# Kernel optimization log

Measured on AMD Instinct MI355X. Metric: run time of the kernel, lower is better.

The kernel has to match this reference:

```python
import jax, jax.numpy as jnp
import numpy as np

K = 16          # neighbors per node
EPS = 1e-5      # BatchNorm eps
BN_SCALE = 1.0 / np.sqrt(1.0 + EPS)  # eval BN with running mean=0, var=1


def _knn_idx(x, k):
    # x: [B, N, d] -> idx [B, N, k] of k nearest neighbors (self excluded)
    sq = jnp.sum(x * x, axis=-1)                               # [B, N]
    d2 = sq[:, :, None] + sq[:, None, :] - 2.0 * jnp.einsum('bnd,bmd->bnm', x, x)
    n = x.shape[1]
    d2 = jnp.where(jnp.eye(n, dtype=bool)[None], jnp.inf, d2)  # no self loops
    _, idx = jax.lax.top_k(-d2, k)
    return idx


def _edge_conv(x, idx, W, b, g, be):
    # PyG EdgeConv: max_j MLP([x_i, x_j - x_i]); MLP = Linear+BN(eval)+ReLU
    xj = jax.vmap(lambda xb, ib: xb[ib])(x, idx)               # [B, N, k, d]
    xi = x[:, :, None, :]
    m = jnp.concatenate([jnp.broadcast_to(xi, xj.shape), xj - xi], axis=-1)
    h = m @ W + b                                              # [B, N, k, out]
    h = g * (h * BN_SCALE) + be                                # eval BatchNorm
    h = jax.nn.relu(h)
    return jnp.max(h, axis=2)                                  # scatter-max over k


def setup_inputs() -> dict:
    key = jax.random.key(0)
    ks = jax.random.split(key, 16)
    B, N, D, C = 128, 256, 6, 12

    def w(k_, shape, fan_in):
        return (jax.random.normal(k_, shape, jnp.float32) / np.sqrt(fan_in)).astype(jnp.float32)

    inp = {
        'x':   jax.random.normal(ks[0], (B, N, D), jnp.float32),
        'W1':  w(ks[1], (2 * 6, 64), 12),   'b1': jnp.zeros((64,), jnp.float32),
        'g1':  jnp.ones((64,), jnp.float32), 'be1': jnp.zeros((64,), jnp.float32),
        'W2':  w(ks[2], (2 * 64, 128), 128), 'b2': jnp.zeros((128,), jnp.float32),
        'g2':  jnp.ones((128,), jnp.float32), 'be2': jnp.zeros((128,), jnp.float32),
        'W3':  w(ks[3], (2 * 128, 256), 256), 'b3': jnp.zeros((256,), jnp.float32),
        'g3':  jnp.ones((256,), jnp.float32), 'be3': jnp.zeros((256,), jnp.float32),
        'Wf1': w(ks[4], (256, 128), 256),    'bf1': jnp.zeros((128,), jnp.float32),
        'gf':  jnp.ones((128,), jnp.float32), 'bef': jnp.zeros((128,), jnp.float32),
        'Wf2': w(ks[5], (128, C), 128),      'bf2': jnp.zeros((C,), jnp.float32),
    }
    return inp


def reference(x, W1, b1, g1, be1, W2, b2, g2, be2, W3, b3, g3, be3,
              Wf1, bf1, gf, bef, Wf2, bf2):
    h = _edge_conv(x, _knn_idx(x, K), W1, b1, g1, be1)   # [B, N, 64]
    h = _edge_conv(h, _knn_idx(h, K), W2, b2, g2, be2)   # [B, N, 128]
    h = _edge_conv(h, _knn_idx(h, K), W3, b3, g3, be3)   # [B, N, 256]
    p = jnp.max(h, axis=1)                               # global_max_pool [B, 256]
    f = jax.nn.relu(gf * ((p @ Wf1 + bf1) * BN_SCALE) + bef)
    return f @ Wf2 + bf2                                 # [B, num_classes]
```

## Files before the change

kernel.cpp:

```cpp
#include <hip/hip_runtime.h>
#include <cstdint>
#include <cstddef>

#define KNN 16
#define NPTS 256
#define NBATCH 128

static constexpr float BN_SCALE_F = 0.9999950000374997f;

__device__ inline unsigned int f32_ord(float f) {
    unsigned int u = __float_as_uint(f);
    return (u & 0x80000000u) ? ~u : (u | 0x80000000u);
}

__device__ __forceinline__ int wmap(int n) { return n + 4 * (n >> 4); }

template<int D>
__global__ __launch_bounds__(256) void sq_kernel(const float* __restrict__ x,
                                                 float* __restrict__ sq) {
    const int t = blockIdx.x * 256 + threadIdx.x;
    const float* r = x + (size_t)t * D;
    float s = 0.f;
    #pragma unroll
    for (int d = 0; d < D; ++d) s = fmaf(r[d], r[d], s);
    sq[t] = s;
}

template<int D>
__global__ __launch_bounds__(256) void knn_fused_kernel(
        const float* __restrict__ x, const float* __restrict__ sq,
        int* __restrict__ idx) {
    constexpr int KS = (D >= 16) ? 16 : D;
    const int t  = threadIdx.x;
    const int tx = t & 15, ty = t >> 4;
    const int sr = t >> 2, sc = t & 3;
    const int b  = blockIdx.x >> 2;
    const int i0 = (blockIdx.x & 3) * 64;
    const int base = b * NPTS;

    __shared__ float As[KS][68];
    __shared__ float Bs[KS][68];
    __shared__ float d2L[64][65];
    __shared__ unsigned short Mi[64][68];

    unsigned int Lv[16], Li[16];
    #pragma unroll
    for (int q = 0; q < 16; ++q) { Lv[q] = 0xFFFFFFFFu; Li[q] = 0u; }

    for (int jt = 0; jt < 4; ++jt) {
        const int j0 = jt * 64;
        float acc[4][4] = {};
        for (int k0 = 0; k0 < D; k0 += KS) {
            if constexpr (D % 16 == 0) {
                const int r  = t >> 2;
                const int cq = (t & 3) * 4;
                const float4 va = *(const float4*)(x + (size_t)(base + i0 + r) * D + k0 + cq);
                const float4 vb = *(const float4*)(x + (size_t)(base + j0 + r) * D + k0 + cq);
                As[cq + 0][r] = va.x; As[cq + 1][r] = va.y;
                As[cq + 2][r] = va.z; As[cq + 3][r] = va.w;
                Bs[cq + 0][r] = vb.x; Bs[cq + 1][r] = vb.y;
                Bs[cq + 2][r] = vb.z; Bs[cq + 3][r] = vb.w;
            } else {
                for (int e = t; e < 64 * KS; e += 256) {
                    const int r = e / KS, c = e % KS;
                    As[c][r] = x[(size_t)(base + i0 + r) * D + k0 + c];
                    Bs[c][r] = x[(size_t)(base + j0 + r) * D + k0 + c];
                }
            }
            __syncthreads();
            #pragma unroll
            for (int kk = 0; kk < KS; ++kk) {
                const float4 av = *(const float4*)&As[kk][ty * 4];
                const float4 bv = *(const float4*)&Bs[kk][tx * 4];
                const float am[4] = {av.x, av.y, av.z, av.w};
                const float bm[4] = {bv.x, bv.y, bv.z, bv.w};
                #pragma unroll
                for (int m = 0; m < 4; ++m)
                    #pragma unroll
                    for (int n = 0; n < 4; ++n)
                        acc[m][n] = fmaf(am[m], bm[n], acc[m][n]);
            }
            __syncthreads();
        }

        float sqi[4], sqj[4];
        #pragma unroll
        for (int m = 0; m < 4; ++m) {
            sqi[m] = sq[base + i0 + ty * 4 + m];
            sqj[m] = sq[base + j0 + tx * 4 + m];
        }
        #pragma unroll
        for (int m = 0; m < 4; ++m) {
            const int gi = i0 + ty * 4 + m;
            #pragma unroll
            for (int n = 0; n < 4; ++n) {
                float v = (sqi[m] + sqj[n]) - 2.f * acc[m][n];
                if (gi == j0 + tx * 4 + n) v = INFINITY;
                d2L[ty * 4 + m][tx * 4 + n] = v;
            }
        }
        __syncthreads();

        #pragma unroll
        for (int i = 0; i < 16; ++i) {
            const unsigned int v = f32_ord(d2L[sr][sc * 16 + i]);
            const unsigned int j = (unsigned int)(j0 + sc * 16 + i);
            #pragma unroll
            for (int q = 15; q >= 1; --q) {
                const bool a = v < Lv[q];
                const bool c = v < Lv[q - 1];
                Lv[q] = a ? (c ? Lv[q - 1] : v) : Lv[q];
                Li[q] = a ? (c ? Li[q - 1] : j) : Li[q];
            }
            const bool a0 = v < Lv[0];
            Lv[0] = a0 ? v : Lv[0];
            Li[0] = a0 ? j : Li[0];
        }
    }

    __syncthreads();
    #pragma unroll
    for (int q = 0; q < 16; ++q) {
        d2L[sr][sc * 16 + q] = __uint_as_float(Lv[q]);
        Mi[sr][sc * 16 + q]  = (unsigned short)Li[q];
    }
    __syncthreads();

    if (t < 64) {
        const int row = t;
        int h[4];
        unsigned int cv[4], ci[4];
        #pragma unroll
        for (int c = 0; c < 4; ++c) {
            h[c]  = 0;
            cv[c] = __float_as_uint(d2L[row][c * 16]);
            ci[c] = Mi[row][c * 16];
        }
        int outj[16];
        #pragma unroll
        for (int rd = 0; rd < 16; ++rd) {
            unsigned int bv = cv[0], bi = ci[0];
            int bc = 0;
            #pragma unroll
            for (int c = 1; c < 4; ++c) {
                const bool tk = (cv[c] < bv) | ((cv[c] == bv) & (ci[c] < bi));
                bv = tk ? cv[c] : bv;
                bi = tk ? ci[c] : bi;
                bc = tk ? c     : bc;
            }
            outj[rd] = (int)bi;
            #pragma unroll
            for (int c = 0; c < 4; ++c) {
                if (c == bc) {
                    const int hn = h[c] + 1;
                    h[c] = hn;
                    if (hn < 16) {
                        cv[c] = __float_as_uint(d2L[row][c * 16 + hn]);
                        ci[c] = Mi[row][c * 16 + hn];
                    } else {
                        cv[c] = 0xFFFFFFFFu;
                    }
                }
            }
        }
        int4* op = (int4*)(idx + (size_t)(base + i0 + row) * KNN);
        op[0] = make_int4(outj[0],  outj[1],  outj[2],  outj[3]);
        op[1] = make_int4(outj[4],  outj[5],  outj[6],  outj[7]);
        op[2] = make_int4(outj[8],  outj[9],  outj[10], outj[11]);
        op[3] = make_int4(outj[12], outj[13], outj[14], outj[15]);
    }
}

template<int D, int C>
__global__ __launch_bounds__(256) void mlp_gemm_kernel(
        const float* __restrict__ x, const float* __restrict__ W,
        const float* __restrict__ bias, const float* __restrict__ g,
        const float* __restrict__ be,
        float* __restrict__ A, float* __restrict__ Bv) {
    constexpr int BM = 128;
    constexpr int KT = (D >= 16) ? 16 : D;
    const int t  = threadIdx.x;
    const int m0 = blockIdx.x * BM;
    const int n0 = blockIdx.y * 128;
    const int tx = t & 15;
    const int ty = t >> 4;

    __shared__ float Xs[KT][BM + 4];
    __shared__ float Ws[KT][160];

    float acc[8][8] = {};

    for (int k0 = 0; k0 < D; k0 += KT) {
        if constexpr (D % 16 == 0) {
            const int r  = t >> 1;
            const int cq = (t & 1) * 8;
            const float* src = x + (size_t)(m0 + r) * D + k0 + cq;
            const float4 v0 = *(const float4*)(src);
            const float4 v1 = *(const float4*)(src + 4);
            Xs[cq + 0][r] = v0.x; Xs[cq + 1][r] = v0.y;
            Xs[cq + 2][r] = v0.z; Xs[cq + 3][r] = v0.w;
            Xs[cq + 4][r] = v1.x; Xs[cq + 5][r] = v1.y;
            Xs[cq + 6][r] = v1.z; Xs[cq + 7][r] = v1.w;
        } else {
            for (int e = t; e < BM * KT; e += 256) {
                const int r = e / KT, c = e % KT;
                Xs[c][r] = x[(size_t)(m0 + r) * D + k0 + c];
            }
        }
        if constexpr (D % 16 == 0) {
            const int wk = t >> 4;
            const int nq = (t & 15) * 8;
            const int mb = wmap(nq);
            const int gn = n0 + nq;
            const int kr = k0 + wk;
            if (gn < C) {
                const float* pt = W + (size_t)kr * C + gn;
                const float* pb = W + (size_t)(D + kr) * C + gn;
                const float4 t0 = *(const float4*)(pt);
                const float4 t1 = *(const float4*)(pt + 4);
                const float4 b0 = *(const float4*)(pb);
                const float4 b1 = *(const float4*)(pb + 4);
                *(float4*)&Ws[wk][mb]     = make_float4(t0.x - b0.x, t0.y - b0.y,
                                                        t0.z - b0.z, t0.w - b0.w);
                *(float4*)&Ws[wk][mb + 4] = make_float4(t1.x - b1.x, t1.y - b1.y,
                                                        t1.z - b1.z, t1.w - b1.w);
            } else {
                const float* pb = W + (size_t)(D + kr) * C + (gn - C);
                *(float4*)&Ws[wk][mb]     = *(const float4*)(pb);
                *(float4*)&Ws[wk][mb + 4] = *(const float4*)(pb + 4);
            }
        } else {
            for (int e = t; e < KT * 128; e += 256) {
                const int k = e >> 7, n = e & 127;
                const int gn = n0 + n, kr = k0 + k;
                Ws[k][wmap(n)] = (gn < C)
                    ? W[(size_t)kr * C + gn] - W[(size_t)(D + kr) * C + gn]
                    : W[(size_t)(D + kr) * C + (gn - C)];
            }
        }
        __syncthreads();

        const int mc = wmap(tx * 8);
        #pragma unroll
        for (int kk = 0; kk < KT; ++kk) {
            float xm[8], wn[8];
            *(float4*)&xm[0] = *(const float4*)&Xs[kk][ty * 8];
            *(float4*)&xm[4] = *(const float4*)&Xs[kk][ty * 8 + 4];
            *(float4*)&wn[0] = *(const float4*)&Ws[kk][mc];
            *(float4*)&wn[4] = *(const float4*)&Ws[kk][mc + 4];
            #pragma unroll
            for (int m = 0; m < 8; ++m)
                #pragma unroll
                for (int n = 0; n < 8; ++n)
                    acc[m][n] = fmaf(xm[m], wn[n], acc[m][n]);
        }
        __syncthreads();
    }

    const int gn = n0 + tx * 8;
    if (gn < C) {
        float fac[8];
        #pragma unroll
        for (int e = 0; e < 8; ++e) fac[e] = g[gn + e] * BN_SCALE_F;
        #pragma unroll
        for (int m = 0; m < 8; ++m) {
            float o[8];
            #pragma unroll
            for (int e = 0; e < 8; ++e) o[e] = fac[e] * acc[m][e];
            float* dst = A + (size_t)(m0 + ty * 8 + m) * C + gn;
            *(float4*)(dst)     = make_float4(o[0], o[1], o[2], o[3]);
            *(float4*)(dst + 4) = make_float4(o[4], o[5], o[6], o[7]);
        }
    } else {
        const int cb = gn - C;
        float fac[8], bb[8], bee[8];
        #pragma unroll
        for (int e = 0; e < 8; ++e) {
            fac[e] = g[cb + e] * BN_SCALE_F;
            bb[e]  = bias[cb + e];
            bee[e] = be[cb + e];
        }
        #pragma unroll
        for (int m = 0; m < 8; ++m) {
            float o[8];
            #pragma unroll
            for (int e = 0; e < 8; ++e)
                o[e] = fmaf(fac[e], acc[m][e] + bb[e], bee[e]);
            float* dst = Bv + (size_t)(m0 + ty * 8 + m) * C + cb;
            *(float4*)(dst)     = make_float4(o[0], o[1], o[2], o[3]);
            *(float4*)(dst + 4) = make_float4(o[4], o[5], o[6], o[7]);
        }
    }
}

template<int C>
__global__ __launch_bounds__(C) void combine_kernel(
        const float* A, const float* __restrict__ Bv,
        const int* __restrict__ idx, float* out) {
    const int bi = blockIdx.x;
    const int c  = threadIdx.x;
    __shared__ int nbr[KNN];
    if (c < KNN) nbr[c] = idx[(size_t)bi * KNN + c];
    __syncthreads();
    const int b0 = bi & ~255;
    float mx = -INFINITY;
    #pragma unroll
    for (int kk = 0; kk < KNN; ++kk)
        mx = fmaxf(mx, Bv[(size_t)(b0 + nbr[kk]) * C + c]);
    float a = A[(size_t)bi * C + c];
    out[(size_t)bi * C + c] = fmaxf(a + mx, 0.f);
}

__global__ __launch_bounds__(256) void head_kernel(
        const float* __restrict__ h3, const float* __restrict__ Wf1,
        const float* __restrict__ bf1, const float* __restrict__ gf,
        const float* __restrict__ bef, const float* __restrict__ Wf2,
        const float* __restrict__ bf2, float* __restrict__ out) {
    const int b   = blockIdx.x;
    const int tid = threadIdx.x;
    __shared__ float p[256];
    __shared__ float f[128];
    const float* hb = h3 + (size_t)b * NPTS * 256;
    float mx = -INFINITY;
    for (int n = 0; n < NPTS; ++n) mx = fmaxf(mx, hb[(size_t)n * 256 + tid]);
    p[tid] = mx;
    __syncthreads();
    if (tid < 128) {
        float acc = bf1[tid];
        for (int d = 0; d < 256; ++d)
            acc = fmaf(p[d], Wf1[(size_t)d * 128 + tid], acc);
        float v = gf[tid] * (acc * BN_SCALE_F) + bef[tid];
        f[tid] = fmaxf(v, 0.f);
    }
    __syncthreads();
    if (tid < 12) {
        float acc = bf2[tid];
        for (int d = 0; d < 128; ++d)
            acc = fmaf(f[d], Wf2[(size_t)d * 12 + tid], acc);
        out[(size_t)b * 12 + tid] = acc;
    }
}

extern "C" void kernel_launch(void* const* d_in, const int* in_sizes, int n_in,
                              void* d_out, int out_size, void* d_ws, size_t ws_size,
                              hipStream_t stream) {
    const float* x   = (const float*)d_in[0];
    const float* W1  = (const float*)d_in[1];
    const float* b1  = (const float*)d_in[2];
    const float* g1  = (const float*)d_in[3];
    const float* be1 = (const float*)d_in[4];
    const float* W2  = (const float*)d_in[5];
    const float* b2  = (const float*)d_in[6];
    const float* g2  = (const float*)d_in[7];
    const float* be2 = (const float*)d_in[8];
    const float* W3  = (const float*)d_in[9];
    const float* b3  = (const float*)d_in[10];
    const float* g3  = (const float*)d_in[11];
    const float* be3 = (const float*)d_in[12];
    const float* Wf1 = (const float*)d_in[13];
    const float* bf1 = (const float*)d_in[14];
    const float* gf  = (const float*)d_in[15];
    const float* bef = (const float*)d_in[16];
    const float* Wf2 = (const float*)d_in[17];
    const float* bf2 = (const float*)d_in[18];
    float* out = (float*)d_out;

    char* ws = (char*)d_ws;
    const size_t idx_bytes = (size_t)NBATCH * NPTS * KNN * sizeof(int);
    const size_t reg_bytes = (size_t)NBATCH * NPTS * 256 * sizeof(float);
    int*   idx = (int*)ws;
    float* R1  = (float*)(ws + idx_bytes);
    float* R2  = (float*)(ws + idx_bytes + reg_bytes);
    float* R3  = (float*)(ws + idx_bytes + 2 * reg_bytes);
    float* sqb = (float*)(ws + idx_bytes + 3 * reg_bytes);

    const int BN = NBATCH * NPTS;
    const int KNN_GRID = NBATCH * 4;
    const int MB = BN / 128;

    sq_kernel<6><<<BN / 256, 256, 0, stream>>>(x, sqb);
    knn_fused_kernel<6><<<KNN_GRID, 256, 0, stream>>>(x, sqb, idx);
    mlp_gemm_kernel<6, 64><<<dim3(MB, 1), 256, 0, stream>>>(
        x, W1, b1, g1, be1, R1, R2);
    combine_kernel<64><<<BN, 64, 0, stream>>>(R1, R2, idx, R1);

    sq_kernel<64><<<BN / 256, 256, 0, stream>>>(R1, sqb);
    knn_fused_kernel<64><<<KNN_GRID, 256, 0, stream>>>(R1, sqb, idx);
    mlp_gemm_kernel<64, 128><<<dim3(MB, 2), 256, 0, stream>>>(
        R1, W2, b2, g2, be2, R2, R3);
    combine_kernel<128><<<BN, 128, 0, stream>>>(R2, R3, idx, R2);

    sq_kernel<128><<<BN / 256, 256, 0, stream>>>(R2, sqb);
    knn_fused_kernel<128><<<KNN_GRID, 256, 0, stream>>>(R2, sqb, idx);
    mlp_gemm_kernel<128, 256><<<dim3(MB, 4), 256, 0, stream>>>(
        R2, W3, b3, g3, be3, R3, R1);
    combine_kernel<256><<<BN, 256, 0, stream>>>(R3, R1, idx, R3);

    head_kernel<<<NBATCH, 256, 0, stream>>>(R3, Wf1, bf1, gf, bef, Wf2, bf2, out);
}
```

Baseline: 463.3 us.

## Split kNN candidate scan into two halves with a separate merge kernel

Each kNN block now scans only half of the candidate columns, which doubles the grid from 512 to 1024 blocks. Each half writes its sorted top-16 (distance, index) pairs to a scratch buffer that aliases R3. A new merge kernel combines the two sorted lists per point into the final 16 indices. The goal is more parallelism and occupancy on the big GPU, paid for by an extra launch, scratch traffic, and a duplicated per-block tile load and selection cost.

Measured after the change: 494.8 us. 6.8% more time.

```diff
diff --git a/kernel.cpp b/kernel.cpp
--- a/kernel.cpp
+++ b/kernel.cpp
@@ -27,15 +27,17 @@
 }
 
 template<int D>
-__global__ __launch_bounds__(256) void knn_fused_kernel(
+__global__ __launch_bounds__(256) void knn_half_kernel(
         const float* __restrict__ x, const float* __restrict__ sq,
-        int* __restrict__ idx) {
+        uint2* __restrict__ halves) {
     constexpr int KS = (D >= 16) ? 16 : D;
     const int t  = threadIdx.x;
     const int tx = t & 15, ty = t >> 4;
     const int sr = t >> 2, sc = t & 3;
-    const int b  = blockIdx.x >> 2;
-    const int i0 = (blockIdx.x & 3) * 64;
+    const int bx = blockIdx.x;
+    const int half = bx & 1;
+    const int i0   = ((bx >> 1) & 3) * 64;
+    const int b    = bx >> 3;
     const int base = b * NPTS;
 
     __shared__ float As[KS][68];
@@ -47,7 +49,7 @@
     #pragma unroll
     for (int q = 0; q < 16; ++q) { Lv[q] = 0xFFFFFFFFu; Li[q] = 0u; }
 
-    for (int jt = 0; jt < 4; ++jt) {
+    for (int jt = half * 2; jt < half * 2 + 2; ++jt) {
         const int j0 = jt * 64;
         float acc[4][4] = {};
         for (int k0 = 0; k0 < D; k0 += KS) {
@@ -136,7 +138,7 @@
             cv[c] = __float_as_uint(d2L[row][c * 16]);
             ci[c] = Mi[row][c * 16];
         }
-        int outj[16];
+        uint2* op = halves + ((size_t)(base + i0 + row) * 2 + half) * 16;
         #pragma unroll
         for (int rd = 0; rd < 16; ++rd) {
             unsigned int bv = cv[0], bi = ci[0];
@@ -148,7 +150,7 @@
                 bi = tk ? ci[c] : bi;
                 bc = tk ? c     : bc;
             }
-            outj[rd] = (int)bi;
+            op[rd] = make_uint2(bv, bi);
             #pragma unroll
             for (int c = 0; c < 4; ++c) {
                 if (c == bc) {
@@ -163,11 +165,28 @@
                 }
             }
         }
-        int4* op = (int4*)(idx + (size_t)(base + i0 + row) * KNN);
-        op[0] = make_int4(outj[0],  outj[1],  outj[2],  outj[3]);
-        op[1] = make_int4(outj[4],  outj[5],  outj[6],  outj[7]);
-        op[2] = make_int4(outj[8],  outj[9],  outj[10], outj[11]);
-        op[3] = make_int4(outj[12], outj[13], outj[14], outj[15]);
+    }
+}
+
+__global__ __launch_bounds__(256) void knn_merge_kernel(
+        const uint2* __restrict__ halves, int* __restrict__ idx) {
+    const int ig = blockIdx.x * 256 + threadIdx.x;
+    const uint2* A = halves + (size_t)ig * 32;
+    const uint2* B = A + 16;
+    int ha = 0, hb = 0;
+    uint2 a = A[0], c = B[0];
+    int* op = idx + (size_t)ig * KNN;
+    #pragma unroll
+    for (int s = 0; s < 16; ++s) {
+        const bool tb = (c.x < a.x) | ((c.x == a.x) & (c.y < a.y));
+        op[s] = (int)(tb ? c.y : a.y);
+        if (tb) {
+            ++hb;
+            c = (hb < 16) ? B[hb] : make_uint2(0xFFFFFFFFu, 0xFFFFFFFFu);
+        } else {
+            ++ha;
+            a = (ha < 16) ? A[ha] : make_uint2(0xFFFFFFFFu, 0xFFFFFFFFu);
+        }
     }
 }
 
@@ -373,25 +392,30 @@
     float* R2  = (float*)(ws + idx_bytes + reg_bytes);
     float* R3  = (float*)(ws + idx_bytes + 2 * reg_bytes);
     float* sqb = (float*)(ws + idx_bytes + 3 * reg_bytes);
+    uint2* hv  = (uint2*)R3;
 
     const int BN = NBATCH * NPTS;
-    const int KNN_GRID = NBATCH * 4;
+    const int KNN_GRID = NBATCH * 8;
+    const int MRG_GRID = BN / 256;
     const int MB = BN / 128;
 
     sq_kernel<6><<<BN / 256, 256, 0, stream>>>(x, sqb);
-    knn_fused_kernel<6><<<KNN_GRID, 256, 0, stream>>>(x, sqb, idx);
+    knn_half_kernel<6><<<KNN_GRID, 256, 0, stream>>>(x, sqb, hv);
+    knn_merge_kernel<<<MRG_GRID, 256, 0, stream>>>(hv, idx);
     mlp_gemm_kernel<6, 64><<<dim3(MB, 1), 256, 0, stream>>>(
         x, W1, b1, g1, be1, R1, R2);
     combine_kernel<64><<<BN, 64, 0, stream>>>(R1, R2, idx, R1);
 
     sq_kernel<64><<<BN / 256, 256, 0, stream>>>(R1, sqb);
-    knn_fused_kernel<64><<<KNN_GRID, 256, 0, stream>>>(R1, sqb, idx);
+    knn_half_kernel<64><<<KNN_GRID, 256, 0, stream>>>(R1, sqb, hv);
+    knn_merge_kernel<<<MRG_GRID, 256, 0, stream>>>(hv, idx);
     mlp_gemm_kernel<64, 128><<<dim3(MB, 2), 256, 0, stream>>>(
         R1, W2, b2, g2, be2, R2, R3);
     combine_kernel<128><<<BN, 128, 0, stream>>>(R2, R3, idx, R2);
 
     sq_kernel<128><<<BN / 256, 256, 0, stream>>>(R2, sqb);
-    knn_fused_kernel<128><<<KNN_GRID, 256, 0, stream>>>(R2, sqb, idx);
+    knn_half_kernel<128><<<KNN_GRID, 256, 0, stream>>>(R2, sqb, hv);
+    knn_merge_kernel<<<MRG_GRID, 256, 0, stream>>>(hv, idx);
     mlp_gemm_kernel<128, 256><<<dim3(MB, 4), 256, 0, stream>>>(
         R2, W3, b3, g3, be3, R3, R1);
     combine_kernel<256><<<BN, 256, 0, stream>>>(R3, R1, idx, R3);
```

## Restructure kNN top-k into value-only threshold selection over full distance row

Applied to the files above, without the earlier changes.

The kNN kernel now stores the full 64x256 distance tile in shared memory and, instead of 256 threads each running an index-tracking insertion sort, uses 128 threads that keep only the 16 smallest values per half-row with min/max networks. The two halves are merged to find the 16th-smallest threshold, and the indices are recovered by scanning the row for values below and then equal to that threshold. This removes the index bookkeeping and ordered-uint conversion, but it uses far fewer active threads during selection, runs serial per-row scans, and enlarges shared memory (about 74 KB), which can lower occupancy. Output neighbor order is now ascending by index rather than by distance.

New measurement: 534.0 us. 15.3% more time.

```diff
diff --git a/kernel.cpp b/kernel.cpp
--- a/kernel.cpp
+++ b/kernel.cpp
@@ -7,11 +7,6 @@
 #define NBATCH 128
 
 static constexpr float BN_SCALE_F = 0.9999950000374997f;
-
-__device__ inline unsigned int f32_ord(float f) {
-    unsigned int u = __float_as_uint(f);
-    return (u & 0x80000000u) ? ~u : (u | 0x80000000u);
-}
 
 __device__ __forceinline__ int wmap(int n) { return n + 4 * (n >> 4); }
 
@@ -33,19 +28,15 @@
     constexpr int KS = (D >= 16) ? 16 : D;
     const int t  = threadIdx.x;
     const int tx = t & 15, ty = t >> 4;
-    const int sr = t >> 2, sc = t & 3;
     const int b  = blockIdx.x >> 2;
     const int i0 = (blockIdx.x & 3) * 64;
     const int base = b * NPTS;
 
-    __shared__ float As[KS][68];
-    __shared__ float Bs[KS][68];
-    __shared__ float d2L[64][65];
-    __shared__ unsigned short Mi[64][68];
-
-    unsigned int Lv[16], Li[16];
-    #pragma unroll
-    for (int q = 0; q < 16; ++q) { Lv[q] = 0xFFFFFFFFu; Li[q] = 0u; }
+    __shared__ float S[2176 + 64 * 257];
+    float (*As)[68]   = (float (*)[68])(S);
+    float (*Bs)[68]   = (float (*)[68])(S + 1088);
+    float (*LvD)[34]  = (float (*)[34])(S);
+    float (*d2f)[257] = (float (*)[257])(S + 2176);
 
     for (int jt = 0; jt < 4; ++jt) {
         const int j0 = jt * 64;
@@ -96,78 +87,50 @@
             for (int n = 0; n < 4; ++n) {
                 float v = (sqi[m] + sqj[n]) - 2.f * acc[m][n];
                 if (gi == j0 + tx * 4 + n) v = INFINITY;
-                d2L[ty * 4 + m][tx * 4 + n] = v;
-            }
-        }
-        __syncthreads();
-
-        #pragma unroll
-        for (int i = 0; i < 16; ++i) {
-            const unsigned int v = f32_ord(d2L[sr][sc * 16 + i]);
-            const unsigned int j = (unsigned int)(j0 + sc * 16 + i);
-            #pragma unroll
-            for (int q = 15; q >= 1; --q) {
-                const bool a = v < Lv[q];
-                const bool c = v < Lv[q - 1];
-                Lv[q] = a ? (c ? Lv[q - 1] : v) : Lv[q];
-                Li[q] = a ? (c ? Li[q - 1] : j) : Li[q];
-            }
-            const bool a0 = v < Lv[0];
-            Lv[0] = a0 ? v : Lv[0];
-            Li[0] = a0 ? j : Li[0];
-        }
-    }
-
-    __syncthreads();
-    #pragma unroll
-    for (int q = 0; q < 16; ++q) {
-        d2L[sr][sc * 16 + q] = __uint_as_float(Lv[q]);
-        Mi[sr][sc * 16 + q]  = (unsigned short)Li[q];
+                d2f[ty * 4 + m][j0 + tx * 4 + n] = v;
+            }
+        }
+    }
+
+    __syncthreads();
+
+    if (t < 128) {
+        const int row = t >> 1, hf = t & 1;
+        float Lv[16];
+        #pragma unroll
+        for (int q = 0; q < 16; ++q) Lv[q] = INFINITY;
+        const float* dr = &d2f[row][hf * 128];
+        for (int j = 0; j < 128; ++j) {
+            const float v = dr[j];
+            #pragma unroll
+            for (int q = 15; q >= 1; --q)
+                Lv[q] = fminf(fmaxf(v, Lv[q - 1]), Lv[q]);
+            Lv[0] = fminf(Lv[0], v);
+        }
+        #pragma unroll
+        for (int q = 0; q < 16; ++q) LvD[row][hf * 16 + q] = Lv[q];
     }
     __syncthreads();
 
     if (t < 64) {
         const int row = t;
-        int h[4];
-        unsigned int cv[4], ci[4];
-        #pragma unroll
-        for (int c = 0; c < 4; ++c) {
-            h[c]  = 0;
-            cv[c] = __float_as_uint(d2L[row][c * 16]);
-            ci[c] = Mi[row][c * 16];
-        }
-        int outj[16];
-        #pragma unroll
-        for (int rd = 0; rd < 16; ++rd) {
-            unsigned int bv = cv[0], bi = ci[0];
-            int bc = 0;
-            #pragma unroll
-            for (int c = 1; c < 4; ++c) {
-                const bool tk = (cv[c] < bv) | ((cv[c] == bv) & (ci[c] < bi));
-                bv = tk ? cv[c] : bv;
-                bi = tk ? ci[c] : bi;
-                bc = tk ? c     : bc;
-            }
-            outj[rd] = (int)bi;
-            #pragma unroll
-            for (int c = 0; c < 4; ++c) {
-                if (c == bc) {
-                    const int hn = h[c] + 1;
-                    h[c] = hn;
-                    if (hn < 16) {
-                        cv[c] = __float_as_uint(d2L[row][c * 16 + hn]);
-                        ci[c] = Mi[row][c * 16 + hn];
-                    } else {
-                        cv[c] = 0xFFFFFFFFu;
-                    }
-                }
-            }
-        }
-        int4* op = (int4*)(idx + (size_t)(base + i0 + row) * KNN);
-        op[0] = make_int4(outj[0],  outj[1],  outj[2],  outj[3]);
-        op[1] = make_int4(outj[4],  outj[5],  outj[6],  outj[7]);
-        op[2] = make_int4(outj[8],  outj[9],  outj[10], outj[11]);
-        op[3] = make_int4(outj[12], outj[13], outj[14], outj[15]);
+        int ha = 0, hb = 0;
+        float T = INFINITY;
+        #pragma unroll
+        for (int s = 0; s < 16; ++s) {
+            const float a = LvD[row][ha];
+            const float c = LvD[row][16 + hb];
+            if (c < a) { T = c; ++hb; } else { T = a; ++ha; }
+        }
+        int cnt = 0;
+        int* op = idx + (size_t)(base + i0 + row) * KNN;
+        const float* dr = d2f[row];
+        for (int j = 0; j < NPTS; ++j) {
+            if (dr[j] < T) { op[cnt] = j; ++cnt; }
+        }
+        for (int j = 0; j < NPTS; ++j) {
+            if (dr[j] == T && cnt < 16) { op[cnt] = j; ++cnt; }
+        }
     }
 }
 
```
